# Performance work log

Hardware: AMD Instinct MI355X
Metric: run time of the kernel (lower is better)

The kernel has to match this reference:

```python
import jax, jax.numpy as jnp
import numpy as np

N_NODES = 100000
N_EDGES = 1600000
IN_FEATS = 128
HIDDEN = 64
OUT_FEATS = 64
N_LABELS = 8


def setup_inputs() -> dict:
    key = jax.random.key(0)
    ks = jax.random.split(key, 10)
    glorot = lambda k, fi, fo: jax.random.normal(k, (fi, fo), jnp.float32) * jnp.sqrt(2.0 / (fi + fo))
    return {
        "features": jax.random.normal(ks[0], (N_NODES, IN_FEATS), jnp.float32),
        "edge_src": jax.random.randint(ks[1], (N_EDGES,), 0, N_NODES, jnp.int32),
        "edge_dst": jax.random.randint(ks[2], (N_EDGES,), 0, N_NODES, jnp.int32),
        "edge_types": jax.random.randint(ks[3], (N_EDGES,), 0, 4, jnp.int32),
        "W1": glorot(ks[4], IN_FEATS, HIDDEN),
        "b1": jnp.zeros((HIDDEN,), jnp.float32),
        "W2": glorot(ks[5], HIDDEN, OUT_FEATS),
        "b2": jnp.zeros((OUT_FEATS,), jnp.float32),
        "Wp": glorot(ks[6], OUT_FEATS, N_LABELS),
        "bp": jnp.zeros((N_LABELS,), jnp.float32),
    }


def _degree_norms(edge_src, edge_dst, n_nodes):
    ones = jnp.ones(edge_src.shape[0], jnp.float32)
    deg_out = jax.ops.segment_sum(ones, edge_src, num_segments=n_nodes)
    deg_in = jax.ops.segment_sum(ones, edge_dst, num_segments=n_nodes)
    # DGL clamps degrees to min 1 before pow(-0.5)
    norm_src = jnp.maximum(deg_out, 1.0) ** -0.5  # [N]
    norm_dst = jnp.maximum(deg_in, 1.0) ** -0.5   # [N]
    return norm_src, norm_dst


def _graph_conv(x, W, b, edge_src, edge_dst, norm_src, norm_dst, n_nodes):
    # norm='both': scale src, dense transform first (mult_first), aggregate, scale dst
    h = (x * norm_src[:, None]) @ W            # [N, out]
    msg = h[edge_src]                          # [E, out] gather
    agg = jax.ops.segment_sum(msg, edge_dst, num_segments=n_nodes)  # [N, out] scatter-add
    return agg * norm_dst[:, None] + b


def reference(features, edge_src, edge_dst, edge_types, W1, b1, W2, b2, Wp, bp):
    n_nodes = features.shape[0]
    norm_src, norm_dst = _degree_norms(edge_src, edge_dst, n_nodes)
    x = jax.nn.relu(_graph_conv(features, W1, b1, edge_src, edge_dst, norm_src, norm_dst, n_nodes))
    # dropout is identity in eval mode
    x = jax.nn.relu(_graph_conv(x, W2, b2, edge_src, edge_dst, norm_src, norm_dst, n_nodes))
    logits = x @ Wp + bp                       # [N, n_labels]
    return jax.nn.softmax(logits, axis=1)
```

## Files before the change

kernel.cpp:

```cpp
#include <hip/hip_runtime.h>
#include <hip/hip_fp16.h>
#include <math.h>


#define NODES   100000
#define INF     128
#define HID     64
#define NLAB    8

#define SB      512
#define NSB     ((NODES + SB - 1) / SB)
#define NHALF   ((NODES + 255) / 256)
#define CAP1    9000
#define SCAP    9000
#define CAP2    4600
#define PCHUNK  4096
#define PEPT    (PCHUNK / 256)
#define SRCMASK 0x1FFFF

#define WCVT_ELEMS (64 * (INF + 8) + 64 * (HID + 8))
#define WCVT_WGS   ((WCVT_ELEMS + 255) / 256)

union H8 { int4 i4; __half2 h2[4]; };

typedef _Float16 half8 __attribute__((ext_vector_type(8)));
typedef float floatx4 __attribute__((ext_vector_type(4)));


__global__ void build1_kernel(const int* __restrict__ src, const int* __restrict__ dst,
                              int* __restrict__ gcur_d, int* __restrict__ gcur_s,
                              int* __restrict__ dreg, unsigned short* __restrict__ sreg,
                              int E, int partWGs,
                              const float* __restrict__ W1, const float* __restrict__ W2,
                              _Float16* __restrict__ wt1, _Float16* __restrict__ wt2) {
    __shared__ int hd[NSB], hs[NSB], bd[NSB], bs[NSB];
    const int tid = threadIdx.x;

    if (blockIdx.x >= partWGs) {
        const int N1 = 64 * (INF + 8);
        const int N2 = 64 * (HID + 8);
        int i = (blockIdx.x - partWGs) * 256 + tid;
        if (i < N1) {
            int n = i / (INF + 8), k = i % (INF + 8);
            wt1[i] = (k < INF) ? (_Float16)W1[k * 64 + n] : (_Float16)0.f;
        } else if (i < N1 + N2) {
            int j = i - N1;
            int n = j / (HID + 8), k = j % (HID + 8);
            wt2[j] = (k < HID) ? (_Float16)W2[k * 64 + n] : (_Float16)0.f;
        }
        return;
    }

    const int e0 = blockIdx.x * PCHUNK;

    for (int i = tid; i < NSB; i += 256) { hd[i] = 0; hs[i] = 0; }
    __syncthreads();

    int es[PEPT], ed[PEPT];
#pragma unroll
    for (int i = 0; i < PEPT; ++i) {
        int e = e0 + tid + i * 256;
        if (e < E) {
            es[i] = src[e]; ed[i] = dst[e];
            atomicAdd(&hd[ed[i] >> 9], 1);
            atomicAdd(&hs[es[i] >> 9], 1);
        } else es[i] = -1;
    }
    __syncthreads();

    for (int b = tid; b < NSB; b += 256) {
        int c = hd[b]; bd[b] = c ? atomicAdd(&gcur_d[b], c) : 0;
        c = hs[b];     bs[b] = c ? atomicAdd(&gcur_s[b], c) : 0;
    }
    __syncthreads();
    for (int b = tid; b < NSB; b += 256) { hd[b] = 0; hs[b] = 0; }
    __syncthreads();

#pragma unroll
    for (int i = 0; i < PEPT; ++i) {
        if (es[i] >= 0) {
            int s = es[i], d = ed[i];
            int kb = d >> 9;
            int pos = bd[kb] + atomicAdd(&hd[kb], 1);
            if (pos < CAP1) dreg[(size_t)kb * CAP1 + pos] = ((d & (SB - 1)) << 17) | s;
            int ks = s >> 9;
            int ps = bs[ks] + atomicAdd(&hs[ks], 1);
            if (ps < SCAP) sreg[(size_t)ks * SCAP + ps] = (unsigned short)(s & (SB - 1));
        }
    }
}


__global__ void shist_kernel(const unsigned short* __restrict__ sreg,
                             const int* __restrict__ gcur_s,
                             float* __restrict__ norm_s, int Nn) {
    __shared__ int hist[SB];
    const int tid = threadIdx.x;
    const int sb = blockIdx.x;
    for (int i = tid; i < SB; i += 256) hist[i] = 0;
    __syncthreads();
    const int cnt = min(gcur_s[sb], SCAP);
    const unsigned short* base = sreg + (size_t)sb * SCAP;
    for (int i = tid; i < cnt; i += 256) atomicAdd(&hist[base[i]], 1);
    __syncthreads();
    for (int t = tid; t < SB; t += 256) {
        int node = sb * SB + t;
        if (node < Nn) norm_s[node] = rsqrtf(fmaxf((float)hist[t], 1.0f));
    }
}


__global__ void build2_kernel(const int* __restrict__ dreg, const int* __restrict__ gcur_d,
                              int* __restrict__ csr, int* __restrict__ starts,
                              int* __restrict__ ends, float* __restrict__ norm_d,
                              const float* __restrict__ Xv, const float* __restrict__ norm,
                              const _Float16* __restrict__ Wt, __half* __restrict__ Hh,
                              int Nn) {
    __shared__ union SMem {
        struct CS { int hist[256]; int excl[256]; int cur[256]; int tot; int sorted[CAP2]; } c;
        _Float16 w[64 * (INF + 8)];
    } sm;
    const int tid = threadIdx.x;

    if (blockIdx.x < NHALF) {
        const int j = blockIdx.x;
        const int sb = j >> 1, half = j & 1;
        const int cnt = min(gcur_d[sb], CAP1);
        const int* reg = dreg + (size_t)sb * CAP1;

        sm.c.hist[tid] = 0;
        __syncthreads();

        for (int i = tid; i < cnt; i += 256) {
            int pe = reg[i];
            if (((pe >> 25) & 1) == half) atomicAdd(&sm.c.hist[(pe >> 17) & 255], 1);
        }
        __syncthreads();

        sm.c.excl[tid] = sm.c.hist[tid];
        __syncthreads();
        for (int off = 1; off < 256; off <<= 1) {
            int v = (tid >= off) ? sm.c.excl[tid - off] : 0;
            __syncthreads();
            sm.c.excl[tid] += v;
            __syncthreads();
        }
        int deg_n = sm.c.hist[tid];
        int st = sm.c.excl[tid] - deg_n;
        if (tid == 255) sm.c.tot = min(sm.c.excl[255], CAP2);
        int node = j * 256 + tid;
        if (node < Nn) {
            int gs = j * CAP2 + st;
            int dcl = min(deg_n, max(CAP2 - st, 0));
            starts[node] = gs;
            ends[node]   = gs + dcl;
            norm_d[node] = rsqrtf(fmaxf((float)deg_n, 1.0f));
        }
        sm.c.cur[tid] = st;
        __syncthreads();

        for (int i = tid; i < cnt; i += 256) {
            int pe = reg[i];
            if (((pe >> 25) & 1) == half) {
                int pos = atomicAdd(&sm.c.cur[(pe >> 17) & 255], 1);
                if (pos < CAP2) sm.c.sorted[pos] = pe & SRCMASK;
            }
        }
        __syncthreads();

        const int tot = sm.c.tot;
        for (int i = tid; i < tot; i += 256) csr[(size_t)j * CAP2 + i] = sm.c.sorted[i];
        return;
    }

    constexpr int K = INF;
    constexpr int KP = K + 8;
    const int bid = blockIdx.x - NHALF;

    constexpr int NI4 = 64 * KP * 2 / 16;
    for (int i = tid; i < NI4; i += 256)
        ((int4*)sm.w)[i] = ((const int4*)Wt)[i];
    __syncthreads();

    const int w = tid >> 6, lane = tid & 63;
    const int m16 = lane & 15, quad = lane >> 4;
    const int rowA = bid * 64 + w * 16 + m16;
    const int rowC = (rowA < Nn) ? rowA : (Nn - 1);

    floatx4 acc0 = {0.f, 0.f, 0.f, 0.f};
    floatx4 acc1 = acc0, acc2 = acc0, acc3 = acc0;

#pragma unroll
    for (int c = 0; c < K / 32; ++c) {
        const int k0 = c * 32 + quad * 8;
        const float* xrow = Xv + (size_t)rowC * K;
        float4 xa = *(const float4*)(xrow + k0);
        float4 xb = *(const float4*)(xrow + k0 + 4);
        half8 a;
        a[0] = (_Float16)xa.x; a[1] = (_Float16)xa.y;
        a[2] = (_Float16)xa.z; a[3] = (_Float16)xa.w;
        a[4] = (_Float16)xb.x; a[5] = (_Float16)xb.y;
        a[6] = (_Float16)xb.z; a[7] = (_Float16)xb.w;
        half8 b0 = *(const half8*)&sm.w[(0 * 16 + m16) * KP + k0];
        half8 b1 = *(const half8*)&sm.w[(1 * 16 + m16) * KP + k0];
        half8 b2 = *(const half8*)&sm.w[(2 * 16 + m16) * KP + k0];
        half8 b3 = *(const half8*)&sm.w[(3 * 16 + m16) * KP + k0];
        acc0 = __builtin_amdgcn_mfma_f32_16x16x32_f16(a, b0, acc0, 0, 0, 0);
        acc1 = __builtin_amdgcn_mfma_f32_16x16x32_f16(a, b1, acc1, 0, 0, 0);
        acc2 = __builtin_amdgcn_mfma_f32_16x16x32_f16(a, b2, acc2, 0, 0, 0);
        acc3 = __builtin_amdgcn_mfma_f32_16x16x32_f16(a, b3, acc3, 0, 0, 0);
    }

    const int rbase = bid * 64 + w * 16 + quad * 4;
    floatx4 accs[4] = {acc0, acc1, acc2, acc3};
#pragma unroll
    for (int i = 0; i < 4; ++i) {
        int grow = rbase + i;
        if (grow < Nn) {
            float nm = norm[grow];
            __half* o = Hh + (size_t)grow * 64 + m16;
#pragma unroll
            for (int t = 0; t < 4; ++t)
                o[16 * t] = (__half)(accs[t][i] * nm);
        }
    }
}


template <int K, bool IN16>
__global__ void gemm_mfma_kernel(const void* __restrict__ Xv, const float* __restrict__ norm,
                                 const _Float16* __restrict__ Wt, __half* __restrict__ Hh,
                                 int M) {
    constexpr int KP = K + 8;
    __shared__ _Float16 sWt[64 * KP];

    const int tid = threadIdx.x;
    constexpr int NI4 = 64 * KP * 2 / 16;
    for (int i = tid; i < NI4; i += 256)
        ((int4*)sWt)[i] = ((const int4*)Wt)[i];
    __syncthreads();

    const int w = tid >> 6, lane = tid & 63;
    const int m16 = lane & 15, quad = lane >> 4;
    const int rowA = blockIdx.x * 64 + w * 16 + m16;
    const int rowC = (rowA < M) ? rowA : (M - 1);

    floatx4 acc0 = {0.f, 0.f, 0.f, 0.f};
    floatx4 acc1 = acc0, acc2 = acc0, acc3 = acc0;

#pragma unroll
    for (int c = 0; c < K / 32; ++c) {
        const int k0 = c * 32 + quad * 8;
        half8 a;
        if constexpr (IN16) {
            const _Float16* xrow = (const _Float16*)Xv + (size_t)rowC * K;
            a = *(const half8*)(xrow + k0);
        } else {
            const float* xrow = (const float*)Xv + (size_t)rowC * K;
            float4 xa = *(const float4*)(xrow + k0);
            float4 xb = *(const float4*)(xrow + k0 + 4);
            a[0] = (_Float16)xa.x; a[1] = (_Float16)xa.y;
            a[2] = (_Float16)xa.z; a[3] = (_Float16)xa.w;
            a[4] = (_Float16)xb.x; a[5] = (_Float16)xb.y;
            a[6] = (_Float16)xb.z; a[7] = (_Float16)xb.w;
        }
        half8 b0 = *(const half8*)&sWt[(0 * 16 + m16) * KP + k0];
        half8 b1 = *(const half8*)&sWt[(1 * 16 + m16) * KP + k0];
        half8 b2 = *(const half8*)&sWt[(2 * 16 + m16) * KP + k0];
        half8 b3 = *(const half8*)&sWt[(3 * 16 + m16) * KP + k0];
        acc0 = __builtin_amdgcn_mfma_f32_16x16x32_f16(a, b0, acc0, 0, 0, 0);
        acc1 = __builtin_amdgcn_mfma_f32_16x16x32_f16(a, b1, acc1, 0, 0, 0);
        acc2 = __builtin_amdgcn_mfma_f32_16x16x32_f16(a, b2, acc2, 0, 0, 0);
        acc3 = __builtin_amdgcn_mfma_f32_16x16x32_f16(a, b3, acc3, 0, 0, 0);
    }

    const int rbase = blockIdx.x * 64 + w * 16 + quad * 4;
    floatx4 accs[4] = {acc0, acc1, acc2, acc3};
#pragma unroll
    for (int i = 0; i < 4; ++i) {
        int grow = rbase + i;
        if (grow < M) {
            float nm = norm[grow];
            __half* o = Hh + (size_t)grow * 64 + m16;
#pragma unroll
            for (int t = 0; t < 4; ++t)
                o[16 * t] = (__half)(accs[t][i] * nm);
        }
    }
}


template <bool PROJ>
__global__ void gather_kernel(const int* __restrict__ starts, const int* __restrict__ ends,
                              const int* __restrict__ csr, const __half* __restrict__ Hh,
                              const float* __restrict__ nd, const float* __restrict__ b,
                              __half* __restrict__ Xh, const float* __restrict__ Wp,
                              const float* __restrict__ bp, float* __restrict__ out,
                              int Nn) {
    __shared__ float sW[NLAB * 65];
    __shared__ float sb_[NLAB];
    const int tid = threadIdx.x;

    if constexpr (PROJ) {
        for (int i = tid; i < 64 * NLAB; i += 256) {
            int k = i >> 3, l = i & 7;
            sW[l * 65 + k] = Wp[i];
        }
        if (tid < NLAB) sb_[tid] = bp[tid];
        __syncthreads();
    }

    const int lane = tid & 63;
    const int half32 = (lane >> 5) & 1;
    const int l32 = lane & 31;
    const int g = l32 >> 3;
    const int c = lane & 7;

    int node = blockIdx.x * 8 + ((tid >> 6) << 1) + half32;
    const bool valid = node < Nn;
    const int nodeC = valid ? node : (Nn - 1);

    const int start = starts[nodeC];
    const int deg   = ends[nodeC] - start;
    const int dmax  = max(deg, __shfl_xor(deg, 32, 64));

    float acc[8] = {0.f, 0.f, 0.f, 0.f, 0.f, 0.f, 0.f, 0.f};

    for (int base = 0; base < dmax; base += 32) {
        int off = base + l32;
        int pe = (off < deg) ? csr[start + off] : 0;
        int ec  = min(deg - base, 32);
        int ecm = min(dmax - base, 32);
        int nkp = (ecm + 7) >> 3;

        for (int k = 0; k < nkp; ++k) {
            int j0 = g + 8 * k;
            int j1 = j0 + 4;
            int s0 = __shfl(pe, (lane & 32) + j0, 64);
            int s1 = __shfl(pe, (lane & 32) + j1, 64);
            H8 v0, v1;
            if (j0 < ec) v0.i4 = ((const int4*)(Hh + (size_t)s0 * 64))[c];
            else         v0.i4 = make_int4(0, 0, 0, 0);
            if (j1 < ec) v1.i4 = ((const int4*)(Hh + (size_t)s1 * 64))[c];
            else         v1.i4 = make_int4(0, 0, 0, 0);
#pragma unroll
            for (int t = 0; t < 4; ++t) {
                __half2 s = __hadd2(v0.h2[t], v1.h2[t]);
                float2 f = __half22float2(s);
                acc[2 * t]     += f.x;
                acc[2 * t + 1] += f.y;
            }
        }
    }

#pragma unroll
    for (int m = 8; m <= 16; m <<= 1) {
#pragma unroll
        for (int k = 0; k < 8; ++k)
            acc[k] += __shfl_xor(acc[k], m, 64);
    }

    if constexpr (!PROJ) {
        if (g == 0 && valid) {
            float nm = nd[node];
            float4 b0 = ((const float4*)b)[2 * c];
            float4 b1 = ((const float4*)b)[2 * c + 1];
            H8 o;
            o.h2[0] = __floats2half2_rn(fmaxf(fmaf(acc[0], nm, b0.x), 0.f),
                                        fmaxf(fmaf(acc[1], nm, b0.y), 0.f));
            o.h2[1] = __floats2half2_rn(fmaxf(fmaf(acc[2], nm, b0.z), 0.f),
                                        fmaxf(fmaf(acc[3], nm, b0.w), 0.f));
            o.h2[2] = __floats2half2_rn(fmaxf(fmaf(acc[4], nm, b1.x), 0.f),
                                        fmaxf(fmaf(acc[5], nm, b1.y), 0.f));
            o.h2[3] = __floats2half2_rn(fmaxf(fmaf(acc[6], nm, b1.z), 0.f),
                                        fmaxf(fmaf(acc[7], nm, b1.w), 0.f));
            ((int4*)(Xh + (size_t)node * 64))[c] = o.i4;
        }
    } else {
        float nm = nd[nodeC];
        float4 b0 = ((const float4*)b)[2 * c];
        float4 b1 = ((const float4*)b)[2 * c + 1];
        float xv[8];
        xv[0] = fmaxf(fmaf(acc[0], nm, b0.x), 0.f);
        xv[1] = fmaxf(fmaf(acc[1], nm, b0.y), 0.f);
        xv[2] = fmaxf(fmaf(acc[2], nm, b0.z), 0.f);
        xv[3] = fmaxf(fmaf(acc[3], nm, b0.w), 0.f);
        xv[4] = fmaxf(fmaf(acc[4], nm, b1.x), 0.f);
        xv[5] = fmaxf(fmaf(acc[5], nm, b1.y), 0.f);
        xv[6] = fmaxf(fmaf(acc[6], nm, b1.z), 0.f);
        xv[7] = fmaxf(fmaf(acc[7], nm, b1.w), 0.f);

        const int l0 = 2 * g, l1 = l0 + 1;
        float p0 = 0.f, p1 = 0.f;
#pragma unroll
        for (int j = 0; j < 8; ++j) {
            p0 = fmaf(xv[j], sW[l0 * 65 + 8 * c + j], p0);
            p1 = fmaf(xv[j], sW[l1 * 65 + 8 * c + j], p1);
        }
        p0 += __shfl_xor(p0, 1, 64); p1 += __shfl_xor(p1, 1, 64);
        p0 += __shfl_xor(p0, 2, 64); p1 += __shfl_xor(p1, 2, 64);
        p0 += __shfl_xor(p0, 4, 64); p1 += __shfl_xor(p1, 4, 64);
        p0 += sb_[l0];
        p1 += sb_[l1];
        float mx = fmaxf(p0, p1);
        mx = fmaxf(mx, __shfl_xor(mx, 8, 64));
        mx = fmaxf(mx, __shfl_xor(mx, 16, 64));
        float e0 = __expf(p0 - mx), e1 = __expf(p1 - mx);
        float s2 = e0 + e1;
        s2 += __shfl_xor(s2, 8, 64);
        s2 += __shfl_xor(s2, 16, 64);
        float inv = 1.0f / s2;
        if (c == 0 && valid) {
            float2 o = {e0 * inv, e1 * inv};
            *(float2*)(out + (size_t)node * NLAB + l0) = o;
        }
    }
}


extern "C" void kernel_launch(void* const* d_in, const int* in_sizes, int n_in,
                              void* d_out, int out_size, void* d_ws, size_t ws_size,
                              hipStream_t stream) {
    const float* features = (const float*)d_in[0];
    const int*   edge_src = (const int*)d_in[1];
    const int*   edge_dst = (const int*)d_in[2];
    const float* W1 = (const float*)d_in[4];
    const float* b1 = (const float*)d_in[5];
    const float* W2 = (const float*)d_in[6];
    const float* b2 = (const float*)d_in[7];
    const float* Wp = (const float*)d_in[8];
    const float* bp = (const float*)d_in[9];
    float* out = (float*)d_out;

    const int N = NODES;
    const int E = in_sizes[1];

    char* p = (char*)d_ws;
    int*   csr    = (int*)p;            p += sizeof(int) * (size_t)NHALF * CAP2;
    int*   starts = (int*)p;            p += sizeof(int) * N;
    int*   ends   = (int*)p;            p += sizeof(int) * N;
    float* norm_s = (float*)p;          p += sizeof(float) * N;
    float* norm_d = (float*)p;          p += sizeof(float) * N;
    int*   gcur_d = (int*)p;            p += sizeof(int) * NSB;
    int*   gcur_s = (int*)p;            p += sizeof(int) * NSB;
    p = (char*)(((size_t)p + 255) & ~(size_t)255);
    _Float16* wt1 = (_Float16*)p;       p += sizeof(_Float16) * 64 * (INF + 8);
    _Float16* wt2 = (_Float16*)p;       p += sizeof(_Float16) * 64 * (HID + 8);
    p = (char*)(((size_t)p + 255) & ~(size_t)255);
    __half* h     = (__half*)p;         p += sizeof(__half) * (size_t)N * 64;
    p = (char*)(((size_t)p + 255) & ~(size_t)255);
    __half* x     = (__half*)p;         p += sizeof(__half) * (size_t)N * 64;
    int*            dreg = (int*)x;
    unsigned short* sreg = (unsigned short*)((char*)x + sizeof(int) * (size_t)NSB * CAP1);

    hipMemsetAsync(gcur_d, 0, sizeof(int) * 2 * NSB, stream);

    const int partWGs = (E + PCHUNK - 1) / PCHUNK;
    build1_kernel<<<partWGs + WCVT_WGS, 256, 0, stream>>>(edge_src, edge_dst,
                                                          gcur_d, gcur_s, dreg, sreg,
                                                          E, partWGs, W1, W2, wt1, wt2);
    shist_kernel<<<NSB, 256, 0, stream>>>(sreg, gcur_s, norm_s, N);
    build2_kernel<<<NHALF + (N + 63) / 64, 256, 0, stream>>>(dreg, gcur_d, csr, starts,
                                                             ends, norm_d,
                                                             features, norm_s, wt1, h, N);

    gather_kernel<false><<<(N + 7) / 8, 256, 0, stream>>>(starts, ends, csr, h, norm_d,
                                                          b1, x, nullptr, nullptr,
                                                          nullptr, N);

    gemm_mfma_kernel<HID, true><<<(N + 63) / 64, 256, 0, stream>>>(x, norm_s, wt2, h, N);
    gather_kernel<true><<<(N + 7) / 8, 256, 0, stream>>>(starts, ends, csr, h, norm_d,
                                                         b2, nullptr, Wp, bp, out, N);
}
```

Baseline: 251.4 us.

## Pad global bucket counters, halve partition chunk, unroll gather loads

The global bucket cursor arrays are padded so each counter sits 64 bytes apart, which is meant to reduce atomic contention and false sharing between neighbouring buckets. The edge partition chunk is halved so more workgroups take part, with fewer edges each. The gather loop now issues four row loads per iteration instead of two and accumulates into float2 vectors, raising memory-level parallelism. Costs are more global atomics from the extra workgroups, higher register pressure in the gather kernel, and a larger counter memset.

```diff
diff --git a/kernel.cpp b/kernel.cpp
--- a/kernel.cpp
+++ b/kernel.cpp
@@ -14,9 +14,10 @@
 #define CAP1    9000
 #define SCAP    9000
 #define CAP2    4600
-#define PCHUNK  4096
+#define PCHUNK  2048
 #define PEPT    (PCHUNK / 256)
 #define SRCMASK 0x1FFFF
+#define GSTRIDE 16
 
 #define WCVT_ELEMS (64 * (INF + 8) + 64 * (HID + 8))
 #define WCVT_WGS   ((WCVT_ELEMS + 255) / 256)
@@ -25,6 +26,7 @@
 
 typedef _Float16 half8 __attribute__((ext_vector_type(8)));
 typedef float floatx4 __attribute__((ext_vector_type(4)));
+typedef float floatx2 __attribute__((ext_vector_type(2)));
 
 
 __global__ void build1_kernel(const int* __restrict__ src, const int* __restrict__ dst,
@@ -69,8 +71,8 @@
     __syncthreads();
 
     for (int b = tid; b < NSB; b += 256) {
-        int c = hd[b]; bd[b] = c ? atomicAdd(&gcur_d[b], c) : 0;
-        c = hs[b];     bs[b] = c ? atomicAdd(&gcur_s[b], c) : 0;
+        int c = hd[b]; bd[b] = c ? atomicAdd(&gcur_d[b * GSTRIDE], c) : 0;
+        c = hs[b];     bs[b] = c ? atomicAdd(&gcur_s[b * GSTRIDE], c) : 0;
     }
     __syncthreads();
     for (int b = tid; b < NSB; b += 256) { hd[b] = 0; hs[b] = 0; }
@@ -99,7 +101,7 @@
     const int sb = blockIdx.x;
     for (int i = tid; i < SB; i += 256) hist[i] = 0;
     __syncthreads();
-    const int cnt = min(gcur_s[sb], SCAP);
+    const int cnt = min(gcur_s[sb * GSTRIDE], SCAP);
     const unsigned short* base = sreg + (size_t)sb * SCAP;
     for (int i = tid; i < cnt; i += 256) atomicAdd(&hist[base[i]], 1);
     __syncthreads();
@@ -125,7 +127,7 @@
     if (blockIdx.x < NHALF) {
         const int j = blockIdx.x;
         const int sb = j >> 1, half = j & 1;
-        const int cnt = min(gcur_d[sb], CAP1);
+        const int cnt = min(gcur_d[sb * GSTRIDE], CAP1);
         const int* reg = dreg + (size_t)sb * CAP1;
 
         sm.c.hist[tid] = 0;
@@ -324,7 +326,7 @@
     const int deg   = ends[nodeC] - start;
     const int dmax  = max(deg, __shfl_xor(deg, 32, 64));
 
-    float acc[8] = {0.f, 0.f, 0.f, 0.f, 0.f, 0.f, 0.f, 0.f};
+    floatx2 acc2[4] = {{0.f, 0.f}, {0.f, 0.f}, {0.f, 0.f}, {0.f, 0.f}};
 
     for (int base = 0; base < dmax; base += 32) {
         int off = base + l32;
@@ -333,22 +335,32 @@
         int ecm = min(dmax - base, 32);
         int nkp = (ecm + 7) >> 3;
 
-        for (int k = 0; k < nkp; ++k) {
+        for (int k = 0; k < nkp; k += 2) {
             int j0 = g + 8 * k;
             int j1 = j0 + 4;
+            int j2 = j0 + 8;
+            int j3 = j0 + 12;
             int s0 = __shfl(pe, (lane & 32) + j0, 64);
             int s1 = __shfl(pe, (lane & 32) + j1, 64);
-            H8 v0, v1;
+            int s2 = __shfl(pe, (lane & 32) + j2, 64);
+            int s3 = __shfl(pe, (lane & 32) + j3, 64);
+            H8 v0, v1, v2, v3;
             if (j0 < ec) v0.i4 = ((const int4*)(Hh + (size_t)s0 * 64))[c];
             else         v0.i4 = make_int4(0, 0, 0, 0);
             if (j1 < ec) v1.i4 = ((const int4*)(Hh + (size_t)s1 * 64))[c];
             else         v1.i4 = make_int4(0, 0, 0, 0);
+            if (j2 < ec) v2.i4 = ((const int4*)(Hh + (size_t)s2 * 64))[c];
+            else         v2.i4 = make_int4(0, 0, 0, 0);
+            if (j3 < ec) v3.i4 = ((const int4*)(Hh + (size_t)s3 * 64))[c];
+            else         v3.i4 = make_int4(0, 0, 0, 0);
 #pragma unroll
             for (int t = 0; t < 4; ++t) {
-                __half2 s = __hadd2(v0.h2[t], v1.h2[t]);
-                float2 f = __half22float2(s);
-                acc[2 * t]     += f.x;
-                acc[2 * t + 1] += f.y;
+                __half2 s01 = __hadd2(v0.h2[t], v1.h2[t]);
+                __half2 s23 = __hadd2(v2.h2[t], v3.h2[t]);
+                floatx2 f01 = {__low2float(s01), __high2float(s01)};
+                floatx2 f23 = {__low2float(s23), __high2float(s23)};
+                acc2[t] += f01;
+                acc2[t] += f23;
             }
         }
     }
@@ -356,8 +368,10 @@
 #pragma unroll
     for (int m = 8; m <= 16; m <<= 1) {
 #pragma unroll
-        for (int k = 0; k < 8; ++k)
-            acc[k] += __shfl_xor(acc[k], m, 64);
+        for (int t = 0; t < 4; ++t) {
+            acc2[t].x += __shfl_xor(acc2[t].x, m, 64);
+            acc2[t].y += __shfl_xor(acc2[t].y, m, 64);
+        }
     }
 
     if constexpr (!PROJ) {
@@ -366,14 +380,14 @@
             float4 b0 = ((const float4*)b)[2 * c];
             float4 b1 = ((const float4*)b)[2 * c + 1];
             H8 o;
-            o.h2[0] = __floats2half2_rn(fmaxf(fmaf(acc[0], nm, b0.x), 0.f),
-                                        fmaxf(fmaf(acc[1], nm, b0.y), 0.f));
-            o.h2[1] = __floats2half2_rn(fmaxf(fmaf(acc[2], nm, b0.z), 0.f),
-                                        fmaxf(fmaf(acc[3], nm, b0.w), 0.f));
-            o.h2[2] = __floats2half2_rn(fmaxf(fmaf(acc[4], nm, b1.x), 0.f),
-                                        fmaxf(fmaf(acc[5], nm, b1.y), 0.f));
-            o.h2[3] = __floats2half2_rn(fmaxf(fmaf(acc[6], nm, b1.z), 0.f),
-                                        fmaxf(fmaf(acc[7], nm, b1.w), 0.f));
+            o.h2[0] = __floats2half2_rn(fmaxf(fmaf(acc2[0].x, nm, b0.x), 0.f),
+                                        fmaxf(fmaf(acc2[0].y, nm, b0.y), 0.f));
+            o.h2[1] = __floats2half2_rn(fmaxf(fmaf(acc2[1].x, nm, b0.z), 0.f),
+                                        fmaxf(fmaf(acc2[1].y, nm, b0.w), 0.f));
+            o.h2[2] = __floats2half2_rn(fmaxf(fmaf(acc2[2].x, nm, b1.x), 0.f),
+                                        fmaxf(fmaf(acc2[2].y, nm, b1.y), 0.f));
+            o.h2[3] = __floats2half2_rn(fmaxf(fmaf(acc2[3].x, nm, b1.z), 0.f),
+                                        fmaxf(fmaf(acc2[3].y, nm, b1.w), 0.f));
             ((int4*)(Xh + (size_t)node * 64))[c] = o.i4;
         }
     } else {
@@ -381,14 +395,14 @@
         float4 b0 = ((const float4*)b)[2 * c];
         float4 b1 = ((const float4*)b)[2 * c + 1];
         float xv[8];
-        xv[0] = fmaxf(fmaf(acc[0], nm, b0.x), 0.f);
-        xv[1] = fmaxf(fmaf(acc[1], nm, b0.y), 0.f);
-        xv[2] = fmaxf(fmaf(acc[2], nm, b0.z), 0.f);
-        xv[3] = fmaxf(fmaf(acc[3], nm, b0.w), 0.f);
-        xv[4] = fmaxf(fmaf(acc[4], nm, b1.x), 0.f);
-        xv[5] = fmaxf(fmaf(acc[5], nm, b1.y), 0.f);
-        xv[6] = fmaxf(fmaf(acc[6], nm, b1.z), 0.f);
-        xv[7] = fmaxf(fmaf(acc[7], nm, b1.w), 0.f);
+        xv[0] = fmaxf(fmaf(acc2[0].x, nm, b0.x), 0.f);
+        xv[1] = fmaxf(fmaf(acc2[0].y, nm, b0.y), 0.f);
+        xv[2] = fmaxf(fmaf(acc2[1].x, nm, b0.z), 0.f);
+        xv[3] = fmaxf(fmaf(acc2[1].y, nm, b0.w), 0.f);
+        xv[4] = fmaxf(fmaf(acc2[2].x, nm, b1.x), 0.f);
+        xv[5] = fmaxf(fmaf(acc2[2].y, nm, b1.y), 0.f);
+        xv[6] = fmaxf(fmaf(acc2[3].x, nm, b1.z), 0.f);
+        xv[7] = fmaxf(fmaf(acc2[3].y, nm, b1.w), 0.f);
 
         const int l0 = 2 * g, l1 = l0 + 1;
         float p0 = 0.f, p1 = 0.f;
@@ -441,8 +455,8 @@
     int*   ends   = (int*)p;            p += sizeof(int) * N;
     float* norm_s = (float*)p;          p += sizeof(float) * N;
     float* norm_d = (float*)p;          p += sizeof(float) * N;
-    int*   gcur_d = (int*)p;            p += sizeof(int) * NSB;
-    int*   gcur_s = (int*)p;            p += sizeof(int) * NSB;
+    int*   gcur_d = (int*)p;            p += sizeof(int) * NSB * GSTRIDE;
+    int*   gcur_s = (int*)p;            p += sizeof(int) * NSB * GSTRIDE;
     p = (char*)(((size_t)p + 255) & ~(size_t)255);
     _Float16* wt1 = (_Float16*)p;       p += sizeof(_Float16) * 64 * (INF + 8);
     _Float16* wt2 = (_Float16*)p;       p += sizeof(_Float16) * 64 * (HID + 8);
@@ -453,7 +467,7 @@
     int*            dreg = (int*)x;
     unsigned short* sreg = (unsigned short*)((char*)x + sizeof(int) * (size_t)NSB * CAP1);
 
-    hipMemsetAsync(gcur_d, 0, sizeof(int) * 2 * NSB, stream);
+    hipMemsetAsync(gcur_d, 0, sizeof(int) * 2 * NSB * GSTRIDE, stream);
 
     const int partWGs = (E + PCHUNK - 1) / PCHUNK;
     build1_kernel<<<partWGs + WCVT_WGS, 256, 0, stream>>>(edge_src, edge_dst,
```

Result: slower. 257.7 us (+2.5%).
